# Kernel tuning notes

Hardware: AMD Instinct MI355X
Metric: run time of the kernel (lower is better)

The kernel has to match this reference:

```python
import jax, jax.numpy as jnp
import numpy as np

LOG2E = 1.44269504

def setup_inputs() -> dict:
    key = jax.random.key(0)
    kq, kk, kv = jax.random.split(key, 3)
    shape = (4, 16, 2048, 128)  # [batch, heads, seq, head_dim]
    return {
        "query": jax.random.normal(kq, shape, dtype=jnp.float32),
        "key": jax.random.normal(kk, shape, dtype=jnp.float32),
        "value": jax.random.normal(kv, shape, dtype=jnp.float32),
    }

def reference(query, key, value):
    head_dim = query.shape[-1]
    scale_factor = 1.0 / (head_dim ** 0.5)  # scale=None path in the torch module
    scaled_q = query * (scale_factor * LOG2E)
    # [b,h,s,d] x [b,h,t,d] -> [b,h,s,t]
    attn_scores = jnp.einsum('bhsd,bhtd->bhst', scaled_q, key)
    attn_weights = jax.nn.softmax(attn_scores, axis=-1)
    # [b,h,s,t] x [b,h,t,d] -> [b,h,s,d]
    return jnp.einsum('bhst,bhtd->bhsd', attn_weights, value)
```

## Files before the change

kernel.cpp:

```cpp
#include <hip/hip_runtime.h>
#include <hip/hip_bf16.h>
#include <stdint.h>

typedef short v8s __attribute__((ext_vector_type(8)));
typedef float v16f __attribute__((ext_vector_type(16)));
typedef unsigned int u32;

constexpr int S = 2048, D = 128, KVBLK = 64, NT = S / KVBLK, BH = 64;
constexpr int QW = 32, WAVES = 8, QBLK = QW * WAVES;

#define LOG2E_F 1.44269504f

__device__ __forceinline__ unsigned short f2bf(float x) {
    union { float f; uint32_t u; } v; v.f = x;
    uint32_t r = v.u + 0x7FFFu + ((v.u >> 16) & 1u);
    return (unsigned short)(r >> 16);
}
__device__ __forceinline__ u32 cvtpk(float lo, float hi) {
    u32 r; asm("v_cvt_pk_bf16_f32 %0, %1, %2" : "=v"(r) : "v"(lo), "v"(hi)); return r;
}
__device__ __forceinline__ void gload_lds16(const void* g, void* l) {
    __builtin_amdgcn_global_load_lds(
        (const __attribute__((address_space(1))) unsigned int*)g,
        (__attribute__((address_space(3))) unsigned int*)l, 16, 0, 0);
}

__global__ __launch_bounds__(256)
void prep_kernel(const float* __restrict__ Kg, const float* __restrict__ Vg,
                 short* __restrict__ Kb, short* __restrict__ VtG)
{
    __shared__ __align__(16) short T[D * KVBLK];
    const int bh = blockIdx.y, kv0 = blockIdx.x * KVBLK;
    const int tid = threadIdx.x;
    {
        const float* kp = Kg + ((size_t)bh * S + kv0) * D;
        short* kb = Kb + ((size_t)bh * S + kv0) * D;
        #pragma unroll
        for (int i = 0; i < 4; ++i) {
            int e = (i * 256 + tid) * 8;
            float4 a = *(const float4*)(kp + e), b = *(const float4*)(kp + e + 4);
            v8s t;
            t[0] = f2bf(a.x); t[1] = f2bf(a.y); t[2] = f2bf(a.z); t[3] = f2bf(a.w);
            t[4] = f2bf(b.x); t[5] = f2bf(b.y); t[6] = f2bf(b.z); t[7] = f2bf(b.w);
            *(v8s*)(kb + e) = t;
        }
    }
    {
        const float* vp = Vg + ((size_t)bh * S + kv0) * D;
        const int kv = tid >> 2, dg = tid & 3;
        #pragma unroll
        for (int s4 = 0; s4 < 4; ++s4) {
            float4 a = *(const float4*)(vp + (size_t)kv * D + s4 * 32 + dg * 8);
            float4 b = *(const float4*)(vp + (size_t)kv * D + s4 * 32 + dg * 8 + 4);
            float vv[8] = {a.x, a.y, a.z, a.w, b.x, b.y, b.z, b.w};
            #pragma unroll
            for (int j = 0; j < 8; ++j) {
                int d = s4 * 32 + dg * 8 + j;
                T[d * KVBLK + (kv ^ ((d & 7) << 3))] = (short)f2bf(vv[j]);
            }
        }
        __syncthreads();
        const int s = tid & 7;
        #pragma unroll
        for (int p = 0; p < 4; ++p) {
            int d = p * 32 + (tid >> 3);
            v8s w = *(const v8s*)(&T[d * KVBLK + ((s ^ (d & 7)) << 3)]);
            *(v8s*)(VtG + (size_t)bh * D * S + (size_t)d * S + kv0 + s * 8) = w;
        }
    }
}

__global__ __launch_bounds__(512, 2)
void fattn_kernel(const float* __restrict__ Qg, const short* __restrict__ Kb,
                  const short* __restrict__ Vb, float* __restrict__ Og)
{
    __shared__ __align__(16) short Ks[2][KVBLK * D];
    __shared__ __align__(16) short Vt[2][D * KVBLK];

    const int tid = threadIdx.x, wave = tid >> 6, lane = tid & 63;
    const int l31 = lane & 31, h = lane >> 5;

    const int bid = blockIdx.x;
    const int bh = (bid & 7) | ((bid >> 6) << 3);
    const int qt = (bid >> 3) & 7;
    const int q0 = qt * QBLK + wave * QW;
    const size_t base = (size_t)bh * S * D;

    const float SCALE = LOG2E_F * LOG2E_F * 0.08838834764831845f;

    v8s qf[8];
    {
        const float* qp = Qg + base + (size_t)(q0 + l31) * D + h * 8;
        #pragma unroll
        for (int kst = 0; kst < 8; ++kst) {
            float4 a = *(const float4*)(qp + kst * 16);
            float4 b = *(const float4*)(qp + kst * 16 + 4);
            union { u32 w[4]; v8s v; } qu;
            qu.w[0] = cvtpk(a.x * SCALE, a.y * SCALE);
            qu.w[1] = cvtpk(a.z * SCALE, a.w * SCALE);
            qu.w[2] = cvtpk(b.x * SCALE, b.y * SCALE);
            qu.w[3] = cvtpk(b.z * SCALE, b.w * SCALE);
            qf[kst] = qu.v;
        }
    }

    v16f o[4];
    #pragma unroll
    for (int i = 0; i < 4; ++i)
        #pragma unroll
        for (int r = 0; r < 16; ++r) o[i][r] = 0.f;
    float m_run = -1e30f, l_run = 0.f;

    auto stage = [&](int buf, int kv0) {
        #pragma unroll
        for (int i = 0; i < 2; ++i) {
            int ch = wave * 2 + i;
            int row = ch * 4 + (lane >> 4);
            int sl = lane & 15;
            const short* src = Kb + base + (size_t)(kv0 + row) * D + ((sl ^ (row & 7)) << 3);
            gload_lds16(src, &Ks[buf][ch * 512]);
        }
        #pragma unroll
        for (int i = 0; i < 2; ++i) {
            int ch = wave * 2 + i;
            int d = ch * 8 + (lane >> 3);
            int sl = lane & 7;
            const short* src = Vb + base + (size_t)d * S + kv0 + ((sl ^ (d & 7)) << 3);
            gload_lds16(src, &Vt[buf][ch * 512]);
        }
    };

    stage(0, 0);
    __syncthreads();

    for (int it = 0; it < NT; ++it) {
        const int c = it & 1;
        if (it + 1 < NT) stage(c ^ 1, (it + 1) * KVBLK);

        const short* ks = &Ks[c][0];
        const short* vt = &Vt[c][0];

        v16f s0, s1;
        #pragma unroll
        for (int r = 0; r < 16; ++r) { s0[r] = 0.f; s1[r] = 0.f; }
        __builtin_amdgcn_s_setprio(1);
        #pragma unroll
        for (int kst = 0; kst < 8; ++kst) {
            int sl = (kst * 2 + h) ^ (l31 & 7);
            v8s k0 = *(const v8s*)(&ks[l31 * D + sl * 8]);
            s0 = __builtin_amdgcn_mfma_f32_32x32x16_bf16(k0, qf[kst], s0, 0, 0, 0);
            v8s k1 = *(const v8s*)(&ks[(32 + l31) * D + sl * 8]);
            s1 = __builtin_amdgcn_mfma_f32_32x32x16_bf16(k1, qf[kst], s1, 0, 0, 0);
        }
        __builtin_amdgcn_s_setprio(0);

        float tm = s0[0];
        #pragma unroll
        for (int r = 1; r < 16; ++r) tm = fmaxf(tm, s0[r]);
        #pragma unroll
        for (int r = 0; r < 16; ++r) tm = fmaxf(tm, s1[r]);
        tm = fmaxf(tm, __shfl_xor(tm, 32));

        bool skip = __all(tm <= m_run + 8.f);
        if (!skip) {
            float m_new = fmaxf(m_run, tm);
            float alpha = exp2f(m_run - m_new);
            #pragma unroll
            for (int i = 0; i < 4; ++i)
                #pragma unroll
                for (int r = 0; r < 16; ++r) o[i][r] *= alpha;
            l_run *= alpha;
            m_run = m_new;
        }
        float ts = 0.f;
        #pragma unroll
        for (int r = 0; r < 16; ++r) { s0[r] = exp2f(s0[r] - m_run); ts += s0[r]; }
        #pragma unroll
        for (int r = 0; r < 16; ++r) { s1[r] = exp2f(s1[r] - m_run); ts += s1[r]; }
        ts += __shfl_xor(ts, 32);
        l_run += ts;

        v8s pf[4];
        #pragma unroll
        for (int ks2 = 0; ks2 < 4; ++ks2) {
            const v16f& P = (ks2 < 2) ? s0 : s1;
            int rb = (ks2 & 1) * 8;
            u32 a  = cvtpk(P[rb + 0], P[rb + 1]);
            u32 b  = cvtpk(P[rb + 2], P[rb + 3]);
            u32 cc = cvtpk(P[rb + 4], P[rb + 5]);
            u32 dd = cvtpk(P[rb + 6], P[rb + 7]);
            asm volatile("v_permlane32_swap_b32 %0, %1" : "+v"(a), "+v"(cc));
            asm volatile("v_permlane32_swap_b32 %0, %1" : "+v"(b), "+v"(dd));
            union { u32 w[4]; v8s v; } pu;
            pu.w[0] = a; pu.w[1] = b; pu.w[2] = cc; pu.w[3] = dd;
            pf[ks2] = pu.v;
        }

        __builtin_amdgcn_s_setprio(1);
        #pragma unroll
        for (int dt = 0; dt < 4; ++dt) {
            int d = dt * 32 + l31;
            #pragma unroll
            for (int ks2 = 0; ks2 < 4; ++ks2) {
                int sl = (ks2 * 2 + h) ^ (d & 7);
                v8s vf = *(const v8s*)(&vt[d * KVBLK + sl * 8]);
                o[dt] = __builtin_amdgcn_mfma_f32_32x32x16_bf16(vf, pf[ks2], o[dt], 0, 0, 0);
            }
        }
        __builtin_amdgcn_s_setprio(0);

        __syncthreads();
    }

    float inv = 1.f / l_run;
    float* op = Og + base + (size_t)(q0 + l31) * D;
    #pragma unroll
    for (int dt = 0; dt < 4; ++dt)
        #pragma unroll
        for (int g = 0; g < 4; ++g) {
            float4 w;
            w.x = o[dt][g * 4 + 0] * inv; w.y = o[dt][g * 4 + 1] * inv;
            w.z = o[dt][g * 4 + 2] * inv; w.w = o[dt][g * 4 + 3] * inv;
            *(float4*)(op + dt * 32 + g * 8 + 4 * h) = w;
        }
}

extern "C" void kernel_launch(void* const* d_in, const int* in_sizes, int n_in,
                              void* d_out, int out_size, void* d_ws, size_t ws_size,
                              hipStream_t stream) {
    const float* Q = (const float*)d_in[0];
    const float* K = (const float*)d_in[1];
    const float* V = (const float*)d_in[2];
    float* O = (float*)d_out;

    short* Kb  = (short*)d_ws;
    short* VtG = Kb + (size_t)BH * S * D;

    prep_kernel<<<dim3(NT, BH), dim3(256), 0, stream>>>(K, V, Kb, VtG);
    fattn_kernel<<<dim3(BH * 8), dim3(512), 0, stream>>>(Q, Kb, VtG, O);
}
```

Measured before the change: 393.6 us.

## Software-pipeline QK^T of next tile with softmax and PV of current

Restructures the attention loop into a two-stage software pipeline. The QK^T MFMAs for tile t+1 are issued before the softmax and PV of tile t, with K staged one tile ahead of V and two score buffers used in ping-pong, unrolled by two. The aim is to overlap MFMA work with the exp and reduction VALU work. It adds 32+ live registers for the second score set, which may cause spills or cut occupancy under the 512-thread, 2-block launch bounds.

Measured after the change: 375.2 us. -4.7%, faster.

```diff
diff --git a/kernel.cpp b/kernel.cpp
--- a/kernel.cpp
+++ b/kernel.cpp
@@ -111,7 +111,7 @@
         for (int r = 0; r < 16; ++r) o[i][r] = 0.f;
     float m_run = -1e30f, l_run = 0.f;
 
-    auto stage = [&](int buf, int kv0) {
+    auto stageK = [&](int buf, int kv0) {
         #pragma unroll
         for (int i = 0; i < 2; ++i) {
             int ch = wave * 2 + i;
@@ -120,6 +120,8 @@
             const short* src = Kb + base + (size_t)(kv0 + row) * D + ((sl ^ (row & 7)) << 3);
             gload_lds16(src, &Ks[buf][ch * 512]);
         }
+    };
+    auto stageV = [&](int buf, int kv0) {
         #pragma unroll
         for (int i = 0; i < 2; ++i) {
             int ch = wave * 2 + i;
@@ -130,37 +132,28 @@
         }
     };
 
-    stage(0, 0);
-    __syncthreads();
-
-    for (int it = 0; it < NT; ++it) {
-        const int c = it & 1;
-        if (it + 1 < NT) stage(c ^ 1, (it + 1) * KVBLK);
-
-        const short* ks = &Ks[c][0];
-        const short* vt = &Vt[c][0];
-
-        v16f s0, s1;
-        #pragma unroll
-        for (int r = 0; r < 16; ++r) { s0[r] = 0.f; s1[r] = 0.f; }
+    auto QKT = [&](const short* ks, v16f& t0, v16f& t1) {
+        #pragma unroll
+        for (int r = 0; r < 16; ++r) { t0[r] = 0.f; t1[r] = 0.f; }
         __builtin_amdgcn_s_setprio(1);
         #pragma unroll
         for (int kst = 0; kst < 8; ++kst) {
             int sl = (kst * 2 + h) ^ (l31 & 7);
             v8s k0 = *(const v8s*)(&ks[l31 * D + sl * 8]);
-            s0 = __builtin_amdgcn_mfma_f32_32x32x16_bf16(k0, qf[kst], s0, 0, 0, 0);
+            t0 = __builtin_amdgcn_mfma_f32_32x32x16_bf16(k0, qf[kst], t0, 0, 0, 0);
             v8s k1 = *(const v8s*)(&ks[(32 + l31) * D + sl * 8]);
-            s1 = __builtin_amdgcn_mfma_f32_32x32x16_bf16(k1, qf[kst], s1, 0, 0, 0);
+            t1 = __builtin_amdgcn_mfma_f32_32x32x16_bf16(k1, qf[kst], t1, 0, 0, 0);
         }
         __builtin_amdgcn_s_setprio(0);
-
-        float tm = s0[0];
-        #pragma unroll
-        for (int r = 1; r < 16; ++r) tm = fmaxf(tm, s0[r]);
-        #pragma unroll
-        for (int r = 0; r < 16; ++r) tm = fmaxf(tm, s1[r]);
+    };
+
+    auto SMAX = [&](v16f& t0, v16f& t1, v8s* pf) {
+        float tm = t0[0];
+        #pragma unroll
+        for (int r = 1; r < 16; ++r) tm = fmaxf(tm, t0[r]);
+        #pragma unroll
+        for (int r = 0; r < 16; ++r) tm = fmaxf(tm, t1[r]);
         tm = fmaxf(tm, __shfl_xor(tm, 32));
-
         bool skip = __all(tm <= m_run + 8.f);
         if (!skip) {
             float m_new = fmaxf(m_run, tm);
@@ -174,16 +167,14 @@
         }
         float ts = 0.f;
         #pragma unroll
-        for (int r = 0; r < 16; ++r) { s0[r] = exp2f(s0[r] - m_run); ts += s0[r]; }
-        #pragma unroll
-        for (int r = 0; r < 16; ++r) { s1[r] = exp2f(s1[r] - m_run); ts += s1[r]; }
+        for (int r = 0; r < 16; ++r) { t0[r] = exp2f(t0[r] - m_run); ts += t0[r]; }
+        #pragma unroll
+        for (int r = 0; r < 16; ++r) { t1[r] = exp2f(t1[r] - m_run); ts += t1[r]; }
         ts += __shfl_xor(ts, 32);
         l_run += ts;
-
-        v8s pf[4];
         #pragma unroll
         for (int ks2 = 0; ks2 < 4; ++ks2) {
-            const v16f& P = (ks2 < 2) ? s0 : s1;
+            const v16f& P = (ks2 < 2) ? t0 : t1;
             int rb = (ks2 & 1) * 8;
             u32 a  = cvtpk(P[rb + 0], P[rb + 1]);
             u32 b  = cvtpk(P[rb + 2], P[rb + 3]);
@@ -195,7 +186,9 @@
             pu.w[0] = a; pu.w[1] = b; pu.w[2] = cc; pu.w[3] = dd;
             pf[ks2] = pu.v;
         }
-
+    };
+
+    auto PV = [&](const short* vt, const v8s* pf) {
         __builtin_amdgcn_s_setprio(1);
         #pragma unroll
         for (int dt = 0; dt < 4; ++dt) {
@@ -208,9 +201,42 @@
             }
         }
         __builtin_amdgcn_s_setprio(0);
-
+    };
+
+    v16f sA0, sA1, sB0, sB1;
+    v8s pfA[4], pfB[4];
+
+    stageK(0, 0);
+    __syncthreads();
+    stageV(0, 0);
+    stageK(1, KVBLK);
+    QKT(&Ks[0][0], sA0, sA1);
+    __syncthreads();
+
+    #pragma unroll 1
+    for (int tt = 1; tt <= NT - 3; tt += 2) {
+        stageV(tt & 1, tt * KVBLK);
+        stageK((tt + 1) & 1, (tt + 1) * KVBLK);
+        QKT(&Ks[tt & 1][0], sB0, sB1);
+        SMAX(sA0, sA1, pfA);
+        PV(&Vt[(tt - 1) & 1][0], pfA);
         __syncthreads();
-    }
+        const int te = tt + 1;
+        stageV(te & 1, te * KVBLK);
+        stageK((te + 1) & 1, (te + 1) * KVBLK);
+        QKT(&Ks[te & 1][0], sA0, sA1);
+        SMAX(sB0, sB1, pfB);
+        PV(&Vt[(te - 1) & 1][0], pfB);
+        __syncthreads();
+    }
+
+    stageV((NT - 1) & 1, (NT - 1) * KVBLK);
+    QKT(&Ks[(NT - 1) & 1][0], sB0, sB1);
+    SMAX(sA0, sA1, pfA);
+    PV(&Vt[(NT - 2) & 1][0], pfA);
+    __syncthreads();
+    SMAX(sB0, sB1, pfB);
+    PV(&Vt[(NT - 1) & 1][0], pfB);
 
     float inv = 1.f / l_run;
     float* op = Og + base + (size_t)(q0 + l31) * D;
```
